# Performance work log

Hardware: AMD Instinct MI355X
Metric: run time of the kernel (lower is better)

The kernel has to match this reference:

```python
import jax, jax.numpy as jnp
import numpy as np
from jax import lax

DATA_NUM, CNUM, AUG_NUM, LNUM = 64, 6, 4, 3
B, H, W = 16, 512, 512
T_SEL = 0  # fixed aug selection (torch draws np.random.randint at runtime)
EPS = 1e-8
DN = ('NCHW', 'OIHW', 'NCHW')


def setup_inputs() -> dict:
    key = jax.random.key(0)
    ks = jax.random.split(key, 8)
    GLA_img_aug = jax.random.uniform(ks[0], (B, 1, H, W), dtype=jnp.float32)
    lbl = jax.random.randint(ks[1], (B, H, W), 0, CNUM, dtype=jnp.int32)
    index = jax.random.randint(ks[2], (B,), 0, DATA_NUM, dtype=jnp.int32)
    # learned params: Bezier control params (5+2=7 slots, only 0..3 used) and per-(sample,class,aug,layer) tiny conv pairs
    param = jax.random.uniform(ks[3], (DATA_NUM, CNUM, AUG_NUM, LNUM, 7), dtype=jnp.float32)
    w1 = 0.1 * jax.random.normal(ks[4], (DATA_NUM, CNUM, AUG_NUM, LNUM, 4, 1, 3, 3), dtype=jnp.float32)
    b1 = 0.01 * jax.random.normal(ks[5], (DATA_NUM, CNUM, AUG_NUM, LNUM, 4), dtype=jnp.float32)
    w2 = 0.1 * jax.random.normal(ks[6], (DATA_NUM, CNUM, AUG_NUM, LNUM, 1, 4, 3, 3), dtype=jnp.float32)
    b2 = 0.01 * jax.random.normal(ks[7], (DATA_NUM, CNUM, AUG_NUM, LNUM, 1), dtype=jnp.float32)
    return {"GLA_img_aug": GLA_img_aug, "lbl": lbl, "index": index,
            "param": param, "w1": w1, "b1": b1, "w2": w2, "b2": b2}


def _conv_pair(x, w1, b1, w2, b2):
    # x: [1,H,W]; per-sample Conv2d(1,4,3,p=1) -> Conv2d(4,1,3,p=1)
    y = lax.conv_general_dilated(x[None], w1, (1, 1), 'SAME', dimension_numbers=DN) + b1[None, :, None, None]
    y = lax.conv_general_dilated(y, w2, (1, 1), 'SAME', dimension_numbers=DN) + b2[None, :, None, None]
    return y[0]

_conv_batch = jax.vmap(_conv_pair)  # batched over per-sample weights


def _ftransfer(xn, lbl, i, index, param, w1, b1, w2, b2):
    raw = xn                                   # [B,1,H,W]
    mask = (lbl[:, None, :, :] == i)           # [B,1,H,W]
    c = xn * mask
    pp = jax.nn.sigmoid(param[index, i, T_SEL])   # [B,L,7]  (p := sigmoid)
    W1, B1 = w1[index, i, T_SEL], b1[index, i, T_SEL]
    W2, B2 = w2[index, i, T_SEL], b2[index, i, T_SEL]
    for layer in range(LNUM):
        p1 = pp[:, layer, 0][:, None, None, None]
        p2 = pp[:, layer, 1][:, None, None, None]
        p1v = pp[:, layer, 2][:, None, None, None]
        p2v = pp[:, layer, 3][:, None, None, None]
        mix = jax.nn.sigmoid(_conv_batch(raw, W1[:, layer], B1[:, layer], W2[:, layer], B2[:, layer]))
        om = 1.0 - c
        ct = 3.0 * om**2 * c * p1 + 3.0 * om * c**2 * p2 + c**3          # p0=0,  p3=1
        cv = om**3 + 3.0 * om**2 * c * p1v + 3.0 * om * c**2 * p2v       # p0v=1, p3v=0
        c = jnp.clip(ct * mix + cv * (1.0 - mix), 0.0, 1.0)
    # write back only where label == i (equivalent to torch's flag-filtered scatter)
    return jnp.where(mask, c, raw)


def reference(GLA_img_aug, lbl, index, param, w1, b1, w2, b2):
    x = GLA_img_aug
    mn = jnp.min(x, axis=(1, 2, 3), keepdims=True)
    mx = jnp.max(x, axis=(1, 2, 3), keepdims=True)
    scale = mx - mn + EPS
    xn = (x - mn) / scale
    for i in range(CNUM):
        xn = _ftransfer(xn, lbl, i, index, param, w1, b1, w2, b2)
    return xn * scale + mn
```

## Files before the change

### kernel.cpp

```cpp
#include <hip/hip_runtime.h>
#include <stdint.h>

#define HW 512
#define IMG (HW*HW)
#define CNUM_ 6

#define TILE 64
#define HALO 12
#define ST 88
#define SSTR 89
#define NT 512
#define RCAP 256

typedef float f2 __attribute__((ext_vector_type(2)));

#define LTOT 7296

#define OFF_MN 512
#define OFF_SC 528
#define OFF_INV 544
#define RECBASE 1024
#define REC_F 96
#define VARBASE (RECBASE + 96*REC_F)
#define VAR_F 27

__global__ __launch_bounds__(256) void k_minmax(const float4* __restrict__ x, float* __restrict__ wsf){
    int blk = blockIdx.x;
    int base4 = blk * 4096;
    float vmin = 1e30f, vmax = -1e30f;
#pragma unroll
    for (int k = 0; k < 16; k++){
        float4 v = x[base4 + k*256 + threadIdx.x];
        vmin = fminf(vmin, fminf(fminf(v.x, v.y), fminf(v.z, v.w)));
        vmax = fmaxf(vmax, fmaxf(fmaxf(v.x, v.y), fmaxf(v.z, v.w)));
    }
    __shared__ float smn[4], smx[4];
#pragma unroll
    for (int off = 32; off > 0; off >>= 1){
        vmin = fminf(vmin, __shfl_down(vmin, off));
        vmax = fmaxf(vmax, __shfl_down(vmax, off));
    }
    int wv = threadIdx.x >> 6;
    if ((threadIdx.x & 63) == 0){ smn[wv] = vmin; smx[wv] = vmax; }
    __syncthreads();
    if (threadIdx.x == 0){
        wsf[2*blk]     = fminf(fminf(smn[0], smn[1]), fminf(smn[2], smn[3]));
        wsf[2*blk + 1] = fmaxf(fmaxf(smx[0], smx[1]), fmaxf(smx[2], smx[3]));
    }
}

__global__ __launch_bounds__(256) void k_prep(const int* __restrict__ index, const float* __restrict__ param,
                       const float* __restrict__ w1, const float* __restrict__ b1,
                       const float* __restrict__ w2, const float* __restrict__ b2,
                       float* __restrict__ wsf){
    __shared__ float w1s[108], w2s[108], b1s[12], b2s[3], prm[21];
    const int r = blockIdx.x, t = threadIdx.x;
    if (r == 0 && t < 16){
        float mn = 1e30f, mx = -1e30f;
        for (int c = 0; c < 16; c++){
            mn = fminf(mn, wsf[2*(t*16 + c)]);
            mx = fmaxf(mx, wsf[2*(t*16 + c) + 1]);
        }
        float sc = mx - mn + 1e-8f;
        wsf[OFF_MN + t] = mn; wsf[OFF_SC + t] = sc; wsf[OFF_INV + t] = 1.0f / sc;
    }
    const int b = r / 6, i = r % 6;
    const int lb0 = (index[b]*CNUM_ + i) * 12;
    if (t < 108){
        int l = t / 36, j = t % 36;
        w1s[t] = w1[(lb0 + l)*36 + j];
        w2s[t] = w2[(lb0 + l)*36 + j];
    }
    if (t < 12) b1s[t] = b1[(lb0 + t/4)*4 + (t%4)];
    if (t < 3)  b2s[t] = b2[lb0 + t];
    if (t < 21) prm[t] = param[(lb0 + t/7)*7 + (t%7)];
    __syncthreads();
    float* rec = wsf + RECBASE + r*REC_F;
    float* var = wsf + VARBASE + r*9*3*VAR_F;
    for (int u = t; u < 9*3*26; u += 256){
        int kind = u / 78, rem = u % 78, l = rem / 26, e = rem % 26;
        int rowk = kind / 3, colk = kind % 3;
        if (e < 25){
            int ty = e/5 - 2, tx = e%5 - 2;
            float we = 0.f;
            for (int d = 0; d < 9; d++){
                int dy = d/3 - 1, dx = d%3 - 1;
                if ((rowk==0 && dy<0)||(rowk==2 && dy>0)||(colk==0 && dx<0)||(colk==2 && dx>0)) continue;
                int ey = ty - dy, ex = tx - dx;
                if (ey < -1 || ey > 1 || ex < -1 || ex > 1) continue;
                for (int c = 0; c < 4; c++)
                    we += w2s[l*36 + c*9 + d] * w1s[l*36 + c*9 + (ey+1)*3 + (ex+1)];
            }
            var[(kind*3 + l)*VAR_F + e] = we;
            if (kind == 4) rec[l*25 + e] = we;
        } else {
            float be = b2s[l];
            for (int c = 0; c < 4; c++){
                float sw = 0.f;
                for (int d = 0; d < 9; d++){
                    int dy = d/3 - 1, dx = d%3 - 1;
                    if ((rowk==0 && dy<0)||(rowk==2 && dy>0)||(colk==0 && dx<0)||(colk==2 && dx>0)) continue;
                    sw += w2s[l*36 + c*9 + d];
                }
                be += b1s[l*4 + c] * sw;
            }
            var[(kind*3 + l)*VAR_F + 25] = be;
            if (kind == 4) rec[75 + l] = be;
        }
    }
    if (t < 18){
        int l = t / 6, q = t % 6;
        float p1  = 1.f/(1.f + __expf(-prm[l*7 + 0]));
        float p2  = 1.f/(1.f + __expf(-prm[l*7 + 1]));
        float p1v = 1.f/(1.f + __expf(-prm[l*7 + 2]));
        float p2v = 1.f/(1.f + __expf(-prm[l*7 + 3]));
        float v;
        switch (q){
            case 0: v = 3.f*p1; break;
            case 1: v = 3.f*p2 - 6.f*p1; break;
            case 2: v = 1.f + 3.f*p1 - 3.f*p2; break;
            case 3: v = 3.f*p1v - 3.f; break;
            case 4: v = 3.f - 6.f*p1v + 3.f*p2v; break;
            default: v = -1.f + 3.f*p1v - 3.f*p2v; break;
        }
        rec[78 + l*6 + q] = v;
    }
}

__device__ __forceinline__ float bez3(float c, float mix, const float* __restrict__ cf){
    float ct = c * (cf[0] + c * (cf[1] + c * cf[2]));
    float cv = 1.f + c * (cf[3] + c * (cf[4] + c * cf[5]));
    float r = cv + mix * (ct - cv);
    return __builtin_amdgcn_fmed3f(r, 0.f, 1.f);
}

__device__ __forceinline__ void load_taps(const float* __restrict__ s, int pos, float* tp){
    const float* sp0 = s + pos - (2*SSTR + 2);
    const float* sp1 = s + pos + (SSTR - 2);
#pragma unroll
    for (int wy = 0; wy < 3; wy++)
#pragma unroll
    for (int wx = 0; wx < 5; wx++)
        tp[wy*5 + wx] = sp0[wy*SSTR + wx];
#pragma unroll
    for (int wy = 0; wy < 2; wy++)
#pragma unroll
    for (int wx = 0; wx < 5; wx++)
        tp[15 + wy*5 + wx] = sp1[wy*SSTR + wx];
}

__device__ __forceinline__ float proc_px(const float* __restrict__ s, int pos,
                                         const float* __restrict__ rec){
    float tp[25];
    load_taps(s, pos, tp);
    f2 a0 = {rec[75], 0.f};
    f2 a1 = {rec[76], 0.f};
    f2 a2 = {rec[77], 0.f};
#pragma unroll
    for (int e = 0; e < 24; e += 2){
        f2 tv = {tp[e], tp[e+1]};
        f2 w0 = {rec[e],      rec[e+1]};
        f2 w1 = {rec[25 + e], rec[26 + e]};
        f2 w2 = {rec[50 + e], rec[51 + e]};
        a0 += w0 * tv;
        a1 += w1 * tv;
        a2 += w2 * tv;
    }
    float t24 = tp[24];
    float s0 = a0.x + a0.y + rec[24]*t24;
    float s1 = a1.x + a1.y + rec[49]*t24;
    float s2 = a2.x + a2.y + rec[74]*t24;
    float c = tp[12];
    c = bez3(c, 1.0f/(1.0f + __expf(-s0)), rec + 78);
    c = bez3(c, 1.0f/(1.0f + __expf(-s1)), rec + 84);
    c = bez3(c, 1.0f/(1.0f + __expf(-s2)), rec + 90);
    return c;
}

__global__ __launch_bounds__(NT, 6) void k_main(
        const float* __restrict__ x, const int* __restrict__ lbl,
        float* __restrict__ out, const float* __restrict__ wsf){
    __shared__ float s[ST*SSTR];
    __shared__ unsigned short lst[LTOT];
    __shared__ unsigned rlst[RCAP];
    __shared__ int cnt[8];
    const int lin = ((blockIdx.z << 3) + blockIdx.y) * 8 + blockIdx.x;
    const int tile = ((lin & 7) << 7) + (lin >> 3);
    const int bz = tile >> 6, by = (tile >> 3) & 7, bx = tile & 7;
    const int b = bz;
    const int X0 = bx * TILE - HALO, Y0 = by * TILE - HALO;
    const float mn = wsf[OFF_MN + b], sc = wsf[OFF_SC + b], inv = wsf[OFF_INV + b];
    const float mninv = mn * inv;
    const int tid = threadIdx.x;
    const int lane = tid & 63;
    const int sbase = b * IMG;
    const bool edgeblk = (bx == 0) | (bx == 7) | (by == 0) | (by == 7);

    if (tid < 8) cnt[tid] = 0;
    __syncthreads();

    for (int it = 0; it < 16; it++){
        int k = it*NT + tid;
        bool inb = k < ST*ST;
        int ly = k / ST, lx = k % ST;
        int gy = Y0 + ly, gx = X0 + lx;
        bool valid = inb && (unsigned)gy < (unsigned)HW && (unsigned)gx < (unsigned)HW;
        float v = 0.f; int c = 255;
        if (valid){
            int off = sbase + gy*HW + gx;
            v = x[off]*inv - mninv;
            c = lbl[off];
        }
        if (inb) s[ly*SSTR + lx] = v;
        int margin = min(min(lx, ST-1-lx), min(ly, ST-1-ly));
        bool ring = valid && ((gx==0) | (gx==HW-1) | (gy==0) | (gy==HW-1));
        bool mainok = valid && !ring && c < CNUM_ && margin >= 2 + 2*c;
        int ce = mainok ? c : 7;
        unsigned short pos = (unsigned short)(ly*SSTR + lx);

        unsigned long long m0 = __ballot(ce & 1);
        unsigned long long m1 = __ballot(ce & 2);
        unsigned long long m2 = __ballot(ce & 4);
        int basev = 0;
        if (lane < 6){
            unsigned long long mc = ((lane & 1) ? m0 : ~m0)
                                  & ((lane & 2) ? m1 : ~m1)
                                  & ((lane & 4) ? m2 : ~m2);
            int pc = __popcll(mc);
            if (pc) basev = atomicAdd(&cnt[lane], pc);
        }
        int mybase = __shfl(basev, ce < 6 ? ce : 0);
        if (mainok){
            unsigned long long mself = ((ce & 1) ? m0 : ~m0)
                                     & ((ce & 2) ? m1 : ~m1)
                                     & ((ce & 4) ? m2 : ~m2);
            int p = mybase + __popcll(mself & ((1ull << lane) - 1ull));
            int capc = 1536 - (ce << 7);
            int offc = ce * (1600 - (ce << 6));
            if (p < capc) lst[offc + p] = pos;
        }
        if (edgeblk){
            bool ringok = ring && c < CNUM_ && margin >= 2;
            unsigned long long rm = __ballot(ringok);
            if (rm){
                int base = 0;
                if (lane == 0) base = atomicAdd(&cnt[6], __popcll(rm));
                base = __shfl(base, 0);
                if (ringok){
                    int p = base + __popcll(rm & ((1ull << lane) - 1ull));
                    if (p < RCAP) rlst[p] = ((unsigned)c << 16) | pos;
                }
            }
        }
    }
    __syncthreads();
    const int rn = min(cnt[6], RCAP);

#pragma unroll
    for (int cls = 0; cls < CNUM_; cls++){
        const int capc = 1536 - (cls << 7);
        const int offc = cls * (1600 - (cls << 6));
        const float* rec = wsf + RECBASE + (b*CNUM_ + cls)*REC_F;
        const int n = min(cnt[cls], capc);
        const unsigned short* lp = lst + offc;
        const int j0 = tid, j1 = tid + NT, j2 = tid + 2*NT;
        int p0 = 0, p1 = 0, p2 = 0;
        float u0, u1, u2;
        if (j0 < n){ p0 = lp[j0]; u0 = proc_px(s, p0, rec); }
        if (j1 < n){ p1 = lp[j1]; u1 = proc_px(s, p1, rec); }
        if (j2 < n){ p2 = lp[j2]; u2 = proc_px(s, p2, rec); }
        int hav = -1; float rupd = 0.f;
        if (edgeblk && tid < rn){
            unsigned e = rlst[tid];
            int rc = (int)(e >> 16), pos = (int)(e & 0xffff);
            int ly = pos / SSTR, lx = pos % SSTR;
            int margin = min(min(lx, ST-1-lx), min(ly, ST-1-ly));
            if (rc == cls && margin >= 2 + 2*cls){
                int gy = Y0 + ly, gx = X0 + lx;
                int rowk = (gy == 0) ? 0 : ((gy == HW-1) ? 2 : 1);
                int colk = (gx == 0) ? 0 : ((gx == HW-1) ? 2 : 1);
                const float* vb = wsf + VARBASE + ((b*CNUM_ + cls)*9 + rowk*3 + colk)*3*VAR_F;
                float tp[25];
                load_taps(s, pos, tp);
                float c = tp[12];
#pragma unroll
                for (int l = 0; l < 3; l++){
                    float z = vb[l*VAR_F + 25];
#pragma unroll
                    for (int e2 = 0; e2 < 25; e2++) z += vb[l*VAR_F + e2] * tp[e2];
                    c = bez3(c, 1.0f/(1.0f + __expf(-z)), rec + 78 + 6*l);
                }
                rupd = c; hav = pos;
            }
        }
        __syncthreads();
        if (j0 < n) s[p0] = u0;
        if (j1 < n) s[p1] = u1;
        if (j2 < n) s[p2] = u2;
        if (hav >= 0) s[hav] = rupd;
        __syncthreads();
    }

    for (int j = tid; j < TILE*TILE; j += NT){
        int py = j >> 6, px = j & 63;
        int gy = Y0 + HALO + py, gx = X0 + HALO + px;
        out[sbase + gy*HW + gx] = s[(HALO + py)*SSTR + (HALO + px)] * sc + mn;
    }
}

extern "C" void kernel_launch(void* const* d_in, const int* in_sizes, int n_in,
                              void* d_out, int out_size, void* d_ws, size_t ws_size,
                              hipStream_t stream){
    const float* x     = (const float*)d_in[0];
    const int*   lbl   = (const int*)  d_in[1];
    const int*   index = (const int*)  d_in[2];
    const float* param = (const float*)d_in[3];
    const float* w1    = (const float*)d_in[4];
    const float* b1    = (const float*)d_in[5];
    const float* w2    = (const float*)d_in[6];
    const float* b2    = (const float*)d_in[7];
    float* out = (float*)d_out;
    float* wsf = (float*)d_ws;

    k_minmax<<<256, 256, 0, stream>>>((const float4*)x, wsf);
    k_prep<<<96, 256, 0, stream>>>(index, param, w1, b1, w2, b2, wsf);
    dim3 g(8, 8, 16);
    k_main<<<g, NT, 0, stream>>>(x, lbl, out, wsf);
}
```

Before: 168.0 us.

## Split per-class pixel list build into two phases to cut LDS and raise occupancy

```diff
diff --git a/kernel.cpp b/kernel.cpp
--- a/kernel.cpp
+++ b/kernel.cpp
@@ -14,7 +14,7 @@
 
 typedef float f2 __attribute__((ext_vector_type(2)));
 
-#define LTOT 7296
+#define LTOT 3840
 
 #define OFF_MN 512
 #define OFF_SC 528
@@ -177,7 +177,7 @@
     return c;
 }
 
-__global__ __launch_bounds__(NT, 6) void k_main(
+__global__ __launch_bounds__(NT, 8) void k_main(
         const float* __restrict__ x, const int* __restrict__ lbl,
         float* __restrict__ out, const float* __restrict__ wsf){
     __shared__ float s[ST*SSTR];
@@ -214,7 +214,7 @@
         if (inb) s[ly*SSTR + lx] = v;
         int margin = min(min(lx, ST-1-lx), min(ly, ST-1-ly));
         bool ring = valid && ((gx==0) | (gx==HW-1) | (gy==0) | (gy==HW-1));
-        bool mainok = valid && !ring && c < CNUM_ && margin >= 2 + 2*c;
+        bool mainok = valid && !ring && c < 3 && margin >= 2 + 2*c;
         int ce = mainok ? c : 7;
         unsigned short pos = (unsigned short)(ly*SSTR + lx);
 
@@ -222,21 +222,21 @@
         unsigned long long m1 = __ballot(ce & 2);
         unsigned long long m2 = __ballot(ce & 4);
         int basev = 0;
-        if (lane < 6){
+        if (lane < 3){
             unsigned long long mc = ((lane & 1) ? m0 : ~m0)
                                   & ((lane & 2) ? m1 : ~m1)
-                                  & ((lane & 4) ? m2 : ~m2);
+                                  & ~m2;
             int pc = __popcll(mc);
             if (pc) basev = atomicAdd(&cnt[lane], pc);
         }
-        int mybase = __shfl(basev, ce < 6 ? ce : 0);
+        int mybase = __shfl(basev, ce < 3 ? ce : 0);
         if (mainok){
             unsigned long long mself = ((ce & 1) ? m0 : ~m0)
                                      & ((ce & 2) ? m1 : ~m1)
-                                     & ((ce & 4) ? m2 : ~m2);
+                                     & ~m2;
             int p = mybase + __popcll(mself & ((1ull << lane) - 1ull));
-            int capc = 1536 - (ce << 7);
-            int offc = ce * (1600 - (ce << 6));
+            int capc = 1408 - (ce << 7);
+            int offc = ce * (1472 - (ce << 6));
             if (p < capc) lst[offc + p] = pos;
         }
         if (edgeblk){
@@ -258,8 +258,48 @@
 
 #pragma unroll
     for (int cls = 0; cls < CNUM_; cls++){
-        const int capc = 1536 - (cls << 7);
-        const int offc = cls * (1600 - (cls << 6));
+        if (cls == 3){
+            for (int it = 0; it < 11; it++){
+                int k = it*NT + tid;
+                bool inb = k < 72*72;
+                int ly = 8 + k / 72, lx = 8 + k % 72;
+                int gy = Y0 + ly, gx = X0 + lx;
+                bool valid = inb && (unsigned)gy < (unsigned)HW && (unsigned)gx < (unsigned)HW;
+                int c = 255;
+                if (valid) c = lbl[sbase + gy*HW + gx];
+                bool ring = valid && ((gx==0) | (gx==HW-1) | (gy==0) | (gy==HW-1));
+                int margin = min(min(lx, ST-1-lx), min(ly, ST-1-ly));
+                bool mainok = valid && !ring && c >= 3 && c < CNUM_ && margin >= 2 + 2*c;
+                int ce = mainok ? (c - 3) : 7;
+                unsigned short pos = (unsigned short)(ly*SSTR + lx);
+
+                unsigned long long m0 = __ballot(ce & 1);
+                unsigned long long m1 = __ballot(ce & 2);
+                unsigned long long m2 = __ballot(ce & 4);
+                int basev = 0;
+                if (lane < 3){
+                    unsigned long long mc = ((lane & 1) ? m0 : ~m0)
+                                          & ((lane & 2) ? m1 : ~m1)
+                                          & ~m2;
+                    int pc = __popcll(mc);
+                    if (pc) basev = atomicAdd(&cnt[3 + lane], pc);
+                }
+                int mybase = __shfl(basev, ce < 3 ? ce : 0);
+                if (mainok){
+                    unsigned long long mself = ((ce & 1) ? m0 : ~m0)
+                                             & ((ce & 2) ? m1 : ~m1)
+                                             & ~m2;
+                    int p = mybase + __popcll(mself & ((1ull << lane) - 1ull));
+                    int capc = 1056 - 96*ce;
+                    int offc = ce * (1104 - 48*ce);
+                    if (p < capc) lst[offc + p] = pos;
+                }
+            }
+            __syncthreads();
+        }
+        const int d = cls - 3;
+        const int capc = (cls < 3) ? (1408 - (cls << 7)) : (1056 - 96*d);
+        const int offc = (cls < 3) ? (cls * (1472 - (cls << 6))) : (d * (1104 - 48*d));
         const float* rec = wsf + RECBASE + (b*CNUM_ + cls)*REC_F;
         const int n = min(cnt[cls], capc);
         const unsigned short* lp = lst + offc;
```

New measurement: 173.6 us. 1.03x slower.

## Spill class-3..5 pixel lists to global output, raise occupancy, pack Bezier math

Applied to the files above, without the earlier changes.

```diff
diff --git a/kernel.cpp b/kernel.cpp
--- a/kernel.cpp
+++ b/kernel.cpp
@@ -14,7 +14,7 @@
 
 typedef float f2 __attribute__((ext_vector_type(2)));
 
-#define LTOT 7296
+#define LTOT 3840
 
 #define OFF_MN 512
 #define OFF_SC 528
@@ -110,10 +110,10 @@
     }
     if (t < 18){
         int l = t / 6, q = t % 6;
-        float p1  = 1.f/(1.f + __expf(-prm[l*7 + 0]));
-        float p2  = 1.f/(1.f + __expf(-prm[l*7 + 1]));
-        float p1v = 1.f/(1.f + __expf(-prm[l*7 + 2]));
-        float p2v = 1.f/(1.f + __expf(-prm[l*7 + 3]));
+        float p1  = __builtin_amdgcn_rcpf(1.f + __expf(-prm[l*7 + 0]));
+        float p2  = __builtin_amdgcn_rcpf(1.f + __expf(-prm[l*7 + 1]));
+        float p1v = __builtin_amdgcn_rcpf(1.f + __expf(-prm[l*7 + 2]));
+        float p2v = __builtin_amdgcn_rcpf(1.f + __expf(-prm[l*7 + 3]));
         float v;
         switch (q){
             case 0: v = 3.f*p1; break;
@@ -127,6 +127,10 @@
     }
 }
 
+__device__ __forceinline__ float sig1(float z){
+    return __builtin_amdgcn_rcpf(1.f + __expf(-z));
+}
+
 __device__ __forceinline__ float bez3(float c, float mix, const float* __restrict__ cf){
     float ct = c * (cf[0] + c * (cf[1] + c * cf[2]));
     float cv = 1.f + c * (cf[3] + c * (cf[4] + c * cf[5]));
@@ -134,6 +138,24 @@
     return __builtin_amdgcn_fmed3f(r, 0.f, 1.f);
 }
 
+__device__ __forceinline__ f2 splat(float v){ f2 r = {v, v}; return r; }
+
+__device__ __forceinline__ f2 sig2(f2 z){
+    f2 r;
+    r.x = __builtin_amdgcn_rcpf(1.f + __expf(-z.x));
+    r.y = __builtin_amdgcn_rcpf(1.f + __expf(-z.y));
+    return r;
+}
+
+__device__ __forceinline__ f2 bez3p(f2 c, f2 mix, const float* __restrict__ cf){
+    f2 ct = c * (splat(cf[0]) + c * (splat(cf[1]) + c * splat(cf[2])));
+    f2 cv = splat(1.f) + c * (splat(cf[3]) + c * (splat(cf[4]) + c * splat(cf[5])));
+    f2 r = cv + mix * (ct - cv);
+    r.x = __builtin_amdgcn_fmed3f(r.x, 0.f, 1.f);
+    r.y = __builtin_amdgcn_fmed3f(r.y, 0.f, 1.f);
+    return r;
+}
+
 __device__ __forceinline__ void load_taps(const float* __restrict__ s, int pos, float* tp){
     const float* sp0 = s + pos - (2*SSTR + 2);
     const float* sp1 = s + pos + (SSTR - 2);
@@ -149,8 +171,9 @@
         tp[15 + wy*5 + wx] = sp1[wy*SSTR + wx];
 }
 
-__device__ __forceinline__ float proc_px(const float* __restrict__ s, int pos,
-                                         const float* __restrict__ rec){
+__device__ __forceinline__ void conv_px(const float* __restrict__ s, int pos,
+                                        const float* __restrict__ rec,
+                                        float& z0, float& z1, float& z2, float& cc){
     float tp[25];
     load_taps(s, pos, tp);
     f2 a0 = {rec[75], 0.f};
@@ -167,17 +190,17 @@
         a2 += w2 * tv;
     }
     float t24 = tp[24];
-    float s0 = a0.x + a0.y + rec[24]*t24;
-    float s1 = a1.x + a1.y + rec[49]*t24;
-    float s2 = a2.x + a2.y + rec[74]*t24;
-    float c = tp[12];
-    c = bez3(c, 1.0f/(1.0f + __expf(-s0)), rec + 78);
-    c = bez3(c, 1.0f/(1.0f + __expf(-s1)), rec + 84);
-    c = bez3(c, 1.0f/(1.0f + __expf(-s2)), rec + 90);
-    return c;
-}
-
-__global__ __launch_bounds__(NT, 6) void k_main(
+    z0 = a0.x + a0.y + rec[24]*t24;
+    z1 = a1.x + a1.y + rec[49]*t24;
+    z2 = a2.x + a2.y + rec[74]*t24;
+    cc = tp[12];
+}
+
+__device__ __forceinline__ unsigned short* gl_addr(float* out, int sbase, int Y0, int X0, int e){
+    return (unsigned short*)(out + sbase + (Y0 + HALO + (e >> 7))*HW + X0 + HALO) + (e & 127);
+}
+
+__global__ __launch_bounds__(NT, 8) void k_main(
         const float* __restrict__ x, const int* __restrict__ lbl,
         float* __restrict__ out, const float* __restrict__ wsf){
     __shared__ float s[ST*SSTR];
@@ -235,9 +258,16 @@
                                      & ((ce & 2) ? m1 : ~m1)
                                      & ((ce & 4) ? m2 : ~m2);
             int p = mybase + __popcll(mself & ((1ull << lane) - 1ull));
-            int capc = 1536 - (ce << 7);
-            int offc = ce * (1600 - (ce << 6));
-            if (p < capc) lst[offc + p] = pos;
+            if (ce < 3){
+                int capc = 1408 - (ce << 7);
+                int offc = ce * (1472 - (ce << 6));
+                if (p < capc) lst[offc + p] = pos;
+            } else {
+                int d = ce - 3;
+                int capc = 1056 - 96*d;
+                int offc = d * (1104 - 48*d);
+                if (p < capc) *gl_addr(out, sbase, Y0, X0, offc + p) = pos;
+            }
         }
         if (edgeblk){
             bool ringok = ring && c < CNUM_ && margin >= 2;
@@ -256,19 +286,58 @@
     __syncthreads();
     const int rn = min(cnt[6], RCAP);
 
+    unsigned short pf[9];
+#pragma unroll
+    for (int d = 0; d < 3; d++){
+        int capc = 1056 - 96*d;
+        int offc = d * (1104 - 48*d);
+        int nB = min(cnt[3 + d], capc);
+#pragma unroll
+        for (int sl = 0; sl < 3; sl++){
+            int j = tid + sl*NT;
+            unsigned short pv = 0;
+            if (j < nB) pv = *gl_addr(out, sbase, Y0, X0, offc + j);
+            pf[d*3 + sl] = pv;
+        }
+    }
+
 #pragma unroll
     for (int cls = 0; cls < CNUM_; cls++){
-        const int capc = 1536 - (cls << 7);
-        const int offc = cls * (1600 - (cls << 6));
+        const int capc = (cls < 3) ? (1408 - (cls << 7)) : (1056 - 96*(cls - 3));
         const float* rec = wsf + RECBASE + (b*CNUM_ + cls)*REC_F;
         const int n = min(cnt[cls], capc);
-        const unsigned short* lp = lst + offc;
         const int j0 = tid, j1 = tid + NT, j2 = tid + 2*NT;
+        const bool v0 = j0 < n, v1 = j1 < n, v2 = j2 < n;
         int p0 = 0, p1 = 0, p2 = 0;
+        if (cls < 3){
+            const unsigned short* lp = lst + cls * (1472 - (cls << 6));
+            if (v0) p0 = lp[j0];
+            if (v1) p1 = lp[j1];
+            if (v2) p2 = lp[j2];
+        } else {
+            p0 = pf[(cls-3)*3 + 0];
+            p1 = pf[(cls-3)*3 + 1];
+            p2 = pf[(cls-3)*3 + 2];
+        }
+        float z00=0.f, z01=0.f, z02=0.f, cc0=0.f;
+        float z10=0.f, z11=0.f, z12=0.f, cc1=0.f;
         float u0, u1, u2;
-        if (j0 < n){ p0 = lp[j0]; u0 = proc_px(s, p0, rec); }
-        if (j1 < n){ p1 = lp[j1]; u1 = proc_px(s, p1, rec); }
-        if (j2 < n){ p2 = lp[j2]; u2 = proc_px(s, p2, rec); }
+        if (v0) conv_px(s, p0, rec, z00, z01, z02, cc0);
+        if (v1) conv_px(s, p1, rec, z10, z11, z12, cc1);
+        if (v0 | v1){
+            f2 cP = {cc0, cc1};
+            cP = bez3p(cP, sig2((f2){z00, z10}), rec + 78);
+            cP = bez3p(cP, sig2((f2){z01, z11}), rec + 84);
+            cP = bez3p(cP, sig2((f2){z02, z12}), rec + 90);
+            u0 = cP.x; u1 = cP.y;
+        }
+        if (v2){
+            float za, zb, zc, cc;
+            conv_px(s, p2, rec, za, zb, zc, cc);
+            cc = bez3(cc, sig1(za), rec + 78);
+            cc = bez3(cc, sig1(zb), rec + 84);
+            u2 = bez3(cc, sig1(zc), rec + 90);
+        }
         int hav = -1; float rupd = 0.f;
         if (edgeblk && tid < rn){
             unsigned e = rlst[tid];
@@ -288,15 +357,15 @@
                     float z = vb[l*VAR_F + 25];
 #pragma unroll
                     for (int e2 = 0; e2 < 25; e2++) z += vb[l*VAR_F + e2] * tp[e2];
-                    c = bez3(c, 1.0f/(1.0f + __expf(-z)), rec + 78 + 6*l);
+                    c = bez3(c, sig1(z), rec + 78 + 6*l);
                 }
                 rupd = c; hav = pos;
             }
         }
         __syncthreads();
-        if (j0 < n) s[p0] = u0;
-        if (j1 < n) s[p1] = u1;
-        if (j2 < n) s[p2] = u2;
+        if (v0) s[p0] = u0;
+        if (v1) s[p1] = u1;
+        if (v2) s[p2] = u2;
         if (hav >= 0) s[hav] = rupd;
         __syncthreads();
     }
```

After: 170.7 us. Within noise of the previous version (+1.6%).
